# Performance work log

Measured on AMD Instinct MI355X. Metric: run time of the kernel, lower is better.

## Reference

```python
import jax, jax.numpy as jnp
import numpy as np

B, S, D = 4, 2048, 2048
H, DH = 16, 128


def setup_inputs() -> dict:
    key = jax.random.key(0)
    k1, k2, k3, k4, k5 = jax.random.split(key, 5)
    x = jax.random.normal(k1, (B, S, D), dtype=jnp.float32)
    # causal mask, broadcast over heads and batch (module does mask.unsqueeze(0))
    attn_mask = jnp.tril(jnp.ones((S, S), dtype=jnp.int32))
    # torch Linear weights: [out, in]; scaled like default init
    w_qkv = jax.random.normal(k2, (3 * H * DH, D), dtype=jnp.float32) / np.sqrt(D)
    b_qkv = jax.random.normal(k3, (3 * H * DH,), dtype=jnp.float32) * 0.01
    w_out = jax.random.normal(k4, (D, H * DH), dtype=jnp.float32) / np.sqrt(H * DH)
    b_out = jax.random.normal(k5, (D,), dtype=jnp.float32) * 0.01
    return {"x": x, "attn_mask": attn_mask, "w_qkv": w_qkv, "b_qkv": b_qkv,
            "w_out": w_out, "b_out": b_out}


def reference(x, attn_mask, w_qkv, b_qkv, w_out, b_out):
    b, s, d = x.shape
    qkv = x @ w_qkv.T + b_qkv                      # [B,S,3*H*DH]
    qkv = qkv.reshape(b, s, H, 3 * DH)             # per-head contiguous 3*DH slice
    qkv = jnp.transpose(qkv, (2, 0, 1, 3))         # [H,B,S,3*DH]
    q, k, v = jnp.split(qkv, 3, axis=-1)           # each [H,B,S,DH]
    scores = jnp.einsum('hbqd,hbkd->hbqk', q, k) / np.sqrt(DH)
    scores = jnp.where(attn_mask[None, None] == 0, -jnp.inf, scores)
    attn = jax.nn.softmax(scores, axis=-1)         # dropout is identity at eval
    ctx = jnp.einsum('hbqk,hbkd->hbqd', attn, v)   # [H,B,S,DH]
    ctx = jnp.transpose(ctx, (1, 2, 0, 3)).reshape(b, s, H * DH)
    return ctx @ w_out.T + b_out
```

## Files before the change

### kernel.cpp

```cpp
#include <hip/hip_runtime.h>

typedef unsigned short u16;
typedef __bf16 bf16x8 __attribute__((ext_vector_type(8)));
typedef unsigned short u16x8 __attribute__((ext_vector_type(8)));
typedef float f32x4 __attribute__((ext_vector_type(4)));

#define GLDS16(gp, lp)                                                        \
  __builtin_amdgcn_global_load_lds(                                           \
      (const __attribute__((address_space(1))) void*)(gp),                    \
      (__attribute__((address_space(3))) void*)(lp), 16, 0, 0)

__device__ __forceinline__ u16 f2bf(float f) {
  unsigned u = __float_as_uint(f);
  u += 0x7FFFu + ((u >> 16) & 1u);
  return (u16)(u >> 16);
}

__device__ __forceinline__ f32x4 mfma_bf16(bf16x8 a, bf16x8 b, f32x4 c) {
  return __builtin_amdgcn_mfma_f32_16x16x32_bf16(a, b, c, 0, 0, 0);
}

__global__ void cvt_f32_bf16(const float* __restrict__ src,
                             u16* __restrict__ dst, int n8) {
  for (int i = blockIdx.x * blockDim.x + threadIdx.x; i < n8;
       i += gridDim.x * blockDim.x) {
    const float4* sp = (const float4*)src + (size_t)i * 2;
    float4 a = sp[0], b = sp[1];
    u16x8 o;
    o[0] = f2bf(a.x); o[1] = f2bf(a.y); o[2] = f2bf(a.z); o[3] = f2bf(a.w);
    o[4] = f2bf(b.x); o[5] = f2bf(b.y); o[6] = f2bf(b.z); o[7] = f2bf(b.w);
    *((u16x8*)dst + i) = o;
  }
}

template <int OUT_BF16>
__global__ __launch_bounds__(512, 2) void gemm8p(const u16* __restrict__ A,
                                                 const u16* __restrict__ B,
                                                 const float* __restrict__ bias,
                                                 void* __restrict__ Cout,
                                                 int M, int N, int K, int nbm) {
  __shared__ __attribute__((aligned(16))) u16 L[2][4][8192];
  const int t = threadIdx.x, lane = t & 63, w = t >> 6;
  const int l15 = lane & 15, l4 = lane >> 4;
  const int wm = w >> 2, wn = w & 3;

  const int cpx = (int)gridDim.x >> 3;
  const int wg = (int)blockIdx.x;
  const int swz = (wg & 7) * cpx + (wg >> 3);
  const int bm = (swz % nbm) * 256;
  const int bn = (swz / nbm) * 256;

  const size_t aoff = (size_t)(t >> 3) * K + (((t & 7) ^ ((t >> 3) & 7)) << 3);
  const u16* SB[4] = {A + (size_t)bm * K, A + (size_t)(bm + 128) * K,
                      B + (size_t)bn * K, B + (size_t)(bn + 128) * K};
  const int ldst = w << 9;

#define STG(d, s, l, kt)                                                      \
  GLDS16(SB[s] + (size_t)(l) * 64 * K + (size_t)(kt) * 64 + aoff,             \
         &L[d][s][(l) * 4096 + ldst])
#define BAR __builtin_amdgcn_s_barrier()
#define WAITL asm volatile("s_waitcnt lgkmcnt(0)" ::: "memory")

  f32x4 acc[8][4];
  f32x4 z4 = {0.f, 0.f, 0.f, 0.f};
#pragma unroll
  for (int i = 0; i < 8; ++i)
#pragma unroll
    for (int j = 0; j < 4; ++j) acc[i][j] = z4;

  const u16* AH[2] = {&L[0][wm][0], &L[1][wm][0]};
  const u16* BH[2] = {&L[0][2 + (wn >> 1)][0], &L[1][2 + (wn >> 1)][0]};
  const int cb = (wn & 1) * 64;

  bf16x8 af[4][2], bfr[4][2];

  auto rdA = [&](const u16* H, int mh) {
#pragma unroll
    for (int m2 = 0; m2 < 4; ++m2) {
      int ra = mh * 64 + m2 * 16 + l15;
      const u16* p = H + ra * 64;
      af[m2][0] = *(const bf16x8*)(p + ((l4 ^ (ra & 7)) << 3));
      af[m2][1] = *(const bf16x8*)(p + (((4 + l4) ^ (ra & 7)) << 3));
    }
  };
  auto rdB = [&](const u16* H, int nh) {
#pragma unroll
    for (int n2 = 0; n2 < 2; ++n2) {
      int rb = cb + (nh * 2 + n2) * 16 + l15;
      const u16* p = H + rb * 64;
      bfr[nh * 2 + n2][0] = *(const bf16x8*)(p + ((l4 ^ (rb & 7)) << 3));
      bfr[nh * 2 + n2][1] = *(const bf16x8*)(p + (((4 + l4) ^ (rb & 7)) << 3));
    }
  };
  auto mma = [&](int mh, int nh) {
    __builtin_amdgcn_s_setprio(1);
#pragma unroll
    for (int m2 = 0; m2 < 4; ++m2)
#pragma unroll
      for (int n2 = 0; n2 < 2; ++n2) {
        int ai = mh * 4 + m2, bi = nh * 2 + n2;
        acc[ai][bi] = mfma_bf16(af[m2][0], bfr[bi][0], acc[ai][bi]);
        acc[ai][bi] = mfma_bf16(af[m2][1], bfr[bi][1], acc[ai][bi]);
      }
    __builtin_amdgcn_s_setprio(0);
  };

  STG(0, 0, 0, 0); STG(0, 0, 1, 0); STG(0, 1, 0, 0); STG(0, 1, 1, 0);
  STG(0, 2, 0, 0); STG(0, 2, 1, 0); STG(0, 3, 0, 0); STG(0, 3, 1, 0);
  STG(1, 0, 0, 1); STG(1, 1, 0, 1); STG(1, 2, 0, 1); STG(1, 2, 1, 1);
  STG(1, 3, 0, 1); STG(1, 3, 1, 1);
  asm volatile("s_waitcnt vmcnt(0)" ::: "memory");
  BAR;

  const int NI = K >> 7;
  for (int i = 0; i < NI; ++i) {
    const int kt = 2 * i;
    const bool st = (i + 1 < NI);
    rdA(AH[0], 0); rdB(BH[0], 0);
    STG(1, 0, 1, kt + 1); STG(1, 1, 1, kt + 1);
    BAR; WAITL; mma(0, 0); BAR;
    rdB(BH[0], 1);
    if (st) { STG(0, 0, 0, kt + 2); STG(0, 1, 0, kt + 2); }
    BAR; WAITL; mma(0, 1); BAR;
    rdA(AH[0], 1);
    if (st) { STG(0, 2, 0, kt + 2); STG(0, 2, 1, kt + 2); }
    BAR; WAITL; mma(1, 1); BAR;
    if (st) {
      STG(0, 3, 0, kt + 2); STG(0, 3, 1, kt + 2);
      asm volatile("s_waitcnt vmcnt(6)" ::: "memory");
    } else {
      asm volatile("s_waitcnt vmcnt(0)" ::: "memory");
    }
    BAR; mma(1, 0); BAR;
    rdA(AH[1], 0); rdB(BH[1], 0);
    if (st) { STG(0, 0, 1, kt + 2); STG(0, 1, 1, kt + 2); }
    BAR; WAITL; mma(0, 0); BAR;
    rdB(BH[1], 1);
    if (st) { STG(1, 0, 0, kt + 3); STG(1, 1, 0, kt + 3); }
    BAR; WAITL; mma(0, 1); BAR;
    rdA(AH[1], 1);
    if (st) { STG(1, 2, 0, kt + 3); STG(1, 2, 1, kt + 3); }
    BAR; WAITL; mma(1, 1); BAR;
    if (st) {
      STG(1, 3, 0, kt + 3); STG(1, 3, 1, kt + 3);
      asm volatile("s_waitcnt vmcnt(6)" ::: "memory");
    }
    BAR; mma(1, 0); BAR;
  }
#undef STG
#undef BAR
#undef WAITL

  const int cr = l4 * 4;
#pragma unroll
  for (int ni = 0; ni < 4; ++ni) {
    int col = bn + wn * 64 + ni * 16 + l15;
    float bv = bias[col];
#pragma unroll
    for (int mi = 0; mi < 8; ++mi) {
      int row = bm + wm * 128 + mi * 16 + cr;
#pragma unroll
      for (int r = 0; r < 4; ++r) {
        float v = acc[mi][ni][r] + bv;
        if (OUT_BF16)
          ((u16*)Cout)[(size_t)(row + r) * N + col] = f2bf(v);
        else
          ((float*)Cout)[(size_t)(row + r) * N + col] = v;
      }
    }
  }
}

__device__ __forceinline__ int vt_idx(int d, int kk) {
  int swz = (d ^ (d >> 3)) & 7;
  return d * 64 + ((((kk >> 3) ^ swz) << 3) | (kk & 7));
}
__device__ __forceinline__ int ps_idx(int r, int c) {
  return r * 64 + ((((c >> 3) ^ ((r >> 2) & 7)) << 3) | (c & 7));
}

__global__ __launch_bounds__(256, 2) void attn_fwd(const u16* __restrict__ qkv,
                                                   u16* __restrict__ ctx) {
  constexpr int NQ = 6144, SD = 2048;
  __shared__ __attribute__((aligned(16))) u16 Ks[2][64 * 128];
  __shared__ __attribute__((aligned(16))) u16 Vt[2][128 * 64];
  __shared__ __attribute__((aligned(16))) u16 Ps[128 * 64];
  const int t = threadIdx.x, lane = t & 63, w = t >> 6;
  const int l15 = lane & 15, l4 = lane >> 4;
  const int h = blockIdx.y, b = blockIdx.z;
  const size_t rowbase = (size_t)b * 2048;
  const int hq = h * 384;

  const u16* Kg = qkv + (rowbase + (t >> 4)) * NQ + hq + 128 +
                  (((t & 15) ^ ((t >> 4) & 7)) << 3);
  const u16* Vg = qkv + (rowbase + (t & 15)) * NQ + hq + 256 + ((t >> 4) << 3);
  const int vkk = t & 15, vd0 = (t >> 4) << 3;

  const float C = 0.12751879522447905f;
  const float THRC = 62.73592239488341f;

  for (int seg = 0; seg < 2; ++seg) {
    const int qt = (seg == 0) ? (15 - (int)blockIdx.x) : (int)blockIdx.x;
    const int q0 = qt * 128;
    const int nt = 2 * qt + 2;
    const int qr0 = q0 + w * 32 + l4 * 4;

    bf16x8 qf[2][4];
#pragma unroll
    for (int mi = 0; mi < 2; ++mi) {
      const u16* qp =
          qkv + (rowbase + q0 + w * 32 + mi * 16 + l15) * NQ + hq + l4 * 8;
#pragma unroll
      for (int kc = 0; kc < 4; ++kc) qf[mi][kc] = *(const bf16x8*)(qp + kc * 32);
    }

    f32x4 z4 = {0.f, 0.f, 0.f, 0.f};
    f32x4 oacc[2][8];
#pragma unroll
    for (int mi = 0; mi < 2; ++mi)
#pragma unroll
      for (int i = 0; i < 8; ++i) oacc[mi][i] = z4;
    float m_run[2][4], l_run[2][4];
#pragma unroll
    for (int mi = 0; mi < 2; ++mi)
#pragma unroll
      for (int r = 0; r < 4; ++r) { m_run[mi][r] = -3.0e38f; l_run[mi][r] = 0.f; }

    u16x8 vA[4], vB[4];
#pragma unroll
    for (int i = 0; i < 4; ++i)
      GLDS16(Kg + (size_t)(i * 16) * NQ, &Ks[0][i * 2048 + w * 512]);
#pragma unroll
    for (int p = 0; p < 4; ++p)
      vA[p] = *(const u16x8*)(Vg + (size_t)(p * 16) * NQ);
    __syncthreads();
#pragma unroll
    for (int p = 0; p < 4; ++p) {
      int kk = p * 16 + vkk;
#pragma unroll
      for (int j = 0; j < 8; ++j) Vt[0][vt_idx(vd0 + j, kk)] = vA[p][j];
    }
#pragma unroll
    for (int p = 0; p < 4; ++p)
      vA[p] = *(const u16x8*)(Vg + (size_t)(64 + p * 16) * NQ);
    __syncthreads();

    for (int tt = 0; tt < nt; ++tt) {
      const int k0 = tt * 64, cur = tt & 1;
      const int kn = (k0 + 64 < q0 + 64) ? k0 + 64 : q0 + 64;
#pragma unroll
      for (int i = 0; i < 4; ++i)
        GLDS16(Kg + (size_t)(kn + i * 16) * NQ,
               &Ks[cur ^ 1][i * 2048 + w * 512]);
      const int kv = (k0 + 128 < q0 + 64) ? k0 + 128 : q0 + 64;
#pragma unroll
      for (int p = 0; p < 4; ++p)
        vB[p] = *(const u16x8*)(Vg + (size_t)(kv + p * 16) * NQ);

      f32x4 sc[2][4];
#pragma unroll
      for (int mi = 0; mi < 2; ++mi)
#pragma unroll
        for (int nf = 0; nf < 4; ++nf) sc[mi][nf] = z4;
#pragma unroll
      for (int kc = 0; kc < 4; ++kc)
#pragma unroll
        for (int nf = 0; nf < 4; ++nf) {
          int rk = nf * 16 + l15;
          bf16x8 kf = *(const bf16x8*)(&Ks[cur][rk * 128 +
                                              (((kc * 4 + l4) ^ (rk & 7)) << 3)]);
          sc[0][nf] = mfma_bf16(qf[0][kc], kf, sc[0][nf]);
          sc[1][nf] = mfma_bf16(qf[1][kc], kf, sc[1][nf]);
        }
      if (tt + 2 >= nt) {
#pragma unroll
        for (int mi = 0; mi < 2; ++mi)
#pragma unroll
          for (int nf = 0; nf < 4; ++nf) {
            int col = k0 + nf * 16 + l15;
            int qr = qr0 + mi * 16;
#pragma unroll
            for (int r = 0; r < 4; ++r)
              if (col > qr + r) sc[mi][nf][r] = -3.0e38f;
          }
      }
      float mx[2][4];
#pragma unroll
      for (int mi = 0; mi < 2; ++mi)
#pragma unroll
        for (int r = 0; r < 4; ++r)
          mx[mi][r] = fmaxf(fmaxf(sc[mi][0][r], sc[mi][1][r]),
                            fmaxf(sc[mi][2][r], sc[mi][3][r]));
#pragma unroll
      for (int off = 8; off >= 1; off >>= 1)
#pragma unroll
        for (int mi = 0; mi < 2; ++mi)
#pragma unroll
          for (int r = 0; r < 4; ++r)
            mx[mi][r] = fmaxf(mx[mi][r], __shfl_xor(mx[mi][r], off));
      bool upd = false;
#pragma unroll
      for (int mi = 0; mi < 2; ++mi)
#pragma unroll
        for (int r = 0; r < 4; ++r)
          upd |= (mx[mi][r] > m_run[mi][r] + THRC);
      if (__any(upd)) {
#pragma unroll
        for (int mi = 0; mi < 2; ++mi)
#pragma unroll
          for (int r = 0; r < 4; ++r) {
            float mn = fmaxf(m_run[mi][r], mx[mi][r]);
            float cr = exp2f((m_run[mi][r] - mn) * C);
            m_run[mi][r] = mn;
            l_run[mi][r] *= cr;
#pragma unroll
            for (int nf = 0; nf < 8; ++nf) oacc[mi][nf][r] *= cr;
          }
      }
#pragma unroll
      for (int mi = 0; mi < 2; ++mi) {
        float mC[4], sm[4];
#pragma unroll
        for (int r = 0; r < 4; ++r) mC[r] = m_run[mi][r] * C;
#pragma unroll
        for (int nf = 0; nf < 4; ++nf)
#pragma unroll
          for (int r = 0; r < 4; ++r)
            sc[mi][nf][r] = exp2f(fmaf(sc[mi][nf][r], C, -mC[r]));
#pragma unroll
        for (int r = 0; r < 4; ++r)
          sm[r] = (sc[mi][0][r] + sc[mi][1][r]) + (sc[mi][2][r] + sc[mi][3][r]);
#pragma unroll
        for (int off = 8; off >= 1; off >>= 1)
#pragma unroll
          for (int r = 0; r < 4; ++r) sm[r] += __shfl_xor(sm[r], off);
#pragma unroll
        for (int r = 0; r < 4; ++r) l_run[mi][r] += sm[r];
#pragma unroll
        for (int nf = 0; nf < 4; ++nf)
#pragma unroll
          for (int r = 0; r < 4; ++r)
            ((__bf16*)Ps)[ps_idx(w * 32 + mi * 16 + l4 * 4 + r,
                                 nf * 16 + l15)] = (__bf16)sc[mi][nf][r];
      }
#pragma unroll
      for (int p = 0; p < 4; ++p) {
        int kk = p * 16 + vkk;
#pragma unroll
        for (int j = 0; j < 8; ++j) Vt[cur ^ 1][vt_idx(vd0 + j, kk)] = vA[p][j];
      }
#pragma unroll
      for (int kc = 0; kc < 2; ++kc) {
        bf16x8 pf0 =
            *(const bf16x8*)(Ps + ps_idx(w * 32 + l15, kc * 32 + l4 * 8));
        bf16x8 pf1 =
            *(const bf16x8*)(Ps + ps_idx(w * 32 + 16 + l15, kc * 32 + l4 * 8));
#pragma unroll
        for (int nf = 0; nf < 8; ++nf) {
          bf16x8 vf = *(const bf16x8*)(&Vt[cur][vt_idx(nf * 16 + l15,
                                                       kc * 32 + l4 * 8)]);
          oacc[0][nf] = mfma_bf16(pf0, vf, oacc[0][nf]);
          oacc[1][nf] = mfma_bf16(pf1, vf, oacc[1][nf]);
        }
      }
      __syncthreads();
#pragma unroll
      for (int p = 0; p < 4; ++p) vA[p] = vB[p];
    }
#pragma unroll
    for (int mi = 0; mi < 2; ++mi) {
      float inv[4];
#pragma unroll
      for (int r = 0; r < 4; ++r) inv[r] = 1.f / l_run[mi][r];
      u16* cp = ctx + (rowbase + q0 + w * 32 + mi * 16 + l4 * 4) * SD +
                h * 128 + l15;
#pragma unroll
      for (int nf = 0; nf < 8; ++nf)
#pragma unroll
        for (int r = 0; r < 4; ++r)
          ((__bf16*)cp)[(size_t)r * SD + nf * 16] =
              (__bf16)(oacc[mi][nf][r] * inv[r]);
    }
  }
}

extern "C" void kernel_launch(void* const* d_in, const int* in_sizes, int n_in,
                              void* d_out, int out_size, void* d_ws,
                              size_t ws_size, hipStream_t stream) {
  const float* x = (const float*)d_in[0];
  const float* wqkv = (const float*)d_in[2];
  const float* bqkv = (const float*)d_in[3];
  const float* wout = (const float*)d_in[4];
  const float* bout = (const float*)d_in[5];
  float* out = (float*)d_out;
  char* ws = (char*)d_ws;

  u16* xb = (u16*)(ws);
  u16* wqkvb = (u16*)(ws + 33554432);
  u16* woutb = (u16*)(ws + 58720256);
  u16* qkvb = (u16*)(ws + 67108864);
  u16* ctx = xb;

  cvt_f32_bf16<<<2048, 256, 0, stream>>>(x, xb, 16777216 / 8);
  cvt_f32_bf16<<<2048, 256, 0, stream>>>(wqkv, wqkvb, 12582912 / 8);
  cvt_f32_bf16<<<1024, 256, 0, stream>>>(wout, woutb, 4194304 / 8);
  gemm8p<1><<<dim3(32 * 24), 512, 0, stream>>>(xb, wqkvb, bqkv, qkvb, 8192,
                                               6144, 2048, 32);
  attn_fwd<<<dim3(8, 16, 4), 256, 0, stream>>>(qkvb, ctx);
  gemm8p<0><<<dim3(32 * 8), 512, 0, stream>>>(ctx, woutb, bout, out, 8192,
                                              2048, 2048, 32);
}
```

Baseline: 635.7 us.

## Single-buffer attention LDS, one q-tile per block, raise occupancy to three

The attention kernel drops double-buffered K/V shared memory and the async global-to-LDS K load. It now loads K and V through registers and stores them into single LDS buffers with an extra barrier per tile. Each block handles one query tile, longest first, instead of pairing two tiles, so the grid becomes 1024 blocks and launch bounds rise to 3 waves per SIMD. The aim is higher occupancy and better load balance through scheduling, at the cost of less intra-block load/compute overlap and more synchronisation.

```diff
diff --git a/kernel.cpp b/kernel.cpp
--- a/kernel.cpp
+++ b/kernel.cpp
@@ -179,208 +179,212 @@
   return r * 64 + ((((c >> 3) ^ ((r >> 2) & 7)) << 3) | (c & 7));
 }
 
-__global__ __launch_bounds__(256, 2) void attn_fwd(const u16* __restrict__ qkv,
+__global__ __launch_bounds__(256, 3) void attn_fwd(const u16* __restrict__ qkv,
                                                    u16* __restrict__ ctx) {
   constexpr int NQ = 6144, SD = 2048;
-  __shared__ __attribute__((aligned(16))) u16 Ks[2][64 * 128];
-  __shared__ __attribute__((aligned(16))) u16 Vt[2][128 * 64];
+  __shared__ __attribute__((aligned(16))) u16 Ks[64 * 128];
+  __shared__ __attribute__((aligned(16))) u16 Vt[128 * 64];
   __shared__ __attribute__((aligned(16))) u16 Ps[128 * 64];
   const int t = threadIdx.x, lane = t & 63, w = t >> 6;
   const int l15 = lane & 15, l4 = lane >> 4;
-  const int h = blockIdx.y, b = blockIdx.z;
+
+  const int L = (int)blockIdx.x;
+  const int qt = 15 - (L >> 6);
+  const int h = L & 15, b = (L >> 4) & 3;
   const size_t rowbase = (size_t)b * 2048;
   const int hq = h * 384;
-
-  const u16* Kg = qkv + (rowbase + (t >> 4)) * NQ + hq + 128 +
-                  (((t & 15) ^ ((t >> 4) & 7)) << 3);
+  const int q0 = qt * 128;
+  const int nt = 2 * qt + 2;
+  const int qr0 = q0 + w * 32 + l4 * 4;
+
+  const u16* KgR =
+      qkv + (rowbase + (t >> 4)) * NQ + hq + 128 + ((t & 15) << 3);
+  const int krow0 = t >> 4;
+  const int kslot = ((t & 15) ^ ((t >> 4) & 7)) << 3;
   const u16* Vg = qkv + (rowbase + (t & 15)) * NQ + hq + 256 + ((t >> 4) << 3);
   const int vkk = t & 15, vd0 = (t >> 4) << 3;
 
   const float C = 0.12751879522447905f;
   const float THRC = 62.73592239488341f;
 
-  for (int seg = 0; seg < 2; ++seg) {
-    const int qt = (seg == 0) ? (15 - (int)blockIdx.x) : (int)blockIdx.x;
-    const int q0 = qt * 128;
-    const int nt = 2 * qt + 2;
-    const int qr0 = q0 + w * 32 + l4 * 4;
-
-    bf16x8 qf[2][4];
+  bf16x8 qf[2][4];
+#pragma unroll
+  for (int mi = 0; mi < 2; ++mi) {
+    const u16* qp =
+        qkv + (rowbase + q0 + w * 32 + mi * 16 + l15) * NQ + hq + l4 * 8;
+#pragma unroll
+    for (int kc = 0; kc < 4; ++kc) qf[mi][kc] = *(const bf16x8*)(qp + kc * 32);
+  }
+
+  f32x4 z4 = {0.f, 0.f, 0.f, 0.f};
+  f32x4 oacc[2][8];
+#pragma unroll
+  for (int mi = 0; mi < 2; ++mi)
+#pragma unroll
+    for (int i = 0; i < 8; ++i) oacc[mi][i] = z4;
+  float m_run[2][4], l_run[2][4];
+#pragma unroll
+  for (int mi = 0; mi < 2; ++mi)
+#pragma unroll
+    for (int r = 0; r < 4; ++r) { m_run[mi][r] = -3.0e38f; l_run[mi][r] = 0.f; }
+
+  u16x8 kA[4], vA[4];
+#pragma unroll
+  for (int i = 0; i < 4; ++i)
+    kA[i] = *(const u16x8*)(KgR + (size_t)(i * 16) * NQ);
+#pragma unroll
+  for (int p = 0; p < 4; ++p)
+    vA[p] = *(const u16x8*)(Vg + (size_t)(p * 16) * NQ);
+#pragma unroll
+  for (int i = 0; i < 4; ++i)
+    *(u16x8*)(Ks + (i * 16 + krow0) * 128 + kslot) = kA[i];
+#pragma unroll
+  for (int p = 0; p < 4; ++p) {
+    int kk = p * 16 + vkk;
+#pragma unroll
+    for (int j = 0; j < 8; ++j) Vt[vt_idx(vd0 + j, kk)] = vA[p][j];
+  }
+  __syncthreads();
+
+  for (int tt = 0; tt < nt; ++tt) {
+    const int k0 = tt * 64;
+    const bool more = (tt + 1 < nt);
+
+    f32x4 sc[2][4];
+#pragma unroll
+    for (int mi = 0; mi < 2; ++mi)
+#pragma unroll
+      for (int nf = 0; nf < 4; ++nf) sc[mi][nf] = z4;
+#pragma unroll
+    for (int kc = 0; kc < 4; ++kc)
+#pragma unroll
+      for (int nf = 0; nf < 4; ++nf) {
+        int rk = nf * 16 + l15;
+        bf16x8 kf = *(const bf16x8*)(Ks + rk * 128 +
+                                     (((kc * 4 + l4) ^ (rk & 7)) << 3));
+        sc[0][nf] = mfma_bf16(qf[0][kc], kf, sc[0][nf]);
+        sc[1][nf] = mfma_bf16(qf[1][kc], kf, sc[1][nf]);
+      }
+    if (tt + 2 >= nt) {
+#pragma unroll
+      for (int mi = 0; mi < 2; ++mi)
+#pragma unroll
+        for (int nf = 0; nf < 4; ++nf) {
+          int col = k0 + nf * 16 + l15;
+          int qr = qr0 + mi * 16;
+#pragma unroll
+          for (int r = 0; r < 4; ++r)
+            if (col > qr + r) sc[mi][nf][r] = -3.0e38f;
+        }
+    }
+    float mx[2][4];
+#pragma unroll
+    for (int mi = 0; mi < 2; ++mi)
+#pragma unroll
+      for (int r = 0; r < 4; ++r)
+        mx[mi][r] = fmaxf(fmaxf(sc[mi][0][r], sc[mi][1][r]),
+                          fmaxf(sc[mi][2][r], sc[mi][3][r]));
+#pragma unroll
+    for (int off = 8; off >= 1; off >>= 1)
+#pragma unroll
+      for (int mi = 0; mi < 2; ++mi)
+#pragma unroll
+        for (int r = 0; r < 4; ++r)
+          mx[mi][r] = fmaxf(mx[mi][r], __shfl_xor(mx[mi][r], off));
+    bool upd = false;
+#pragma unroll
+    for (int mi = 0; mi < 2; ++mi)
+#pragma unroll
+      for (int r = 0; r < 4; ++r) upd |= (mx[mi][r] > m_run[mi][r] + THRC);
+    if (__any(upd)) {
+#pragma unroll
+      for (int mi = 0; mi < 2; ++mi)
+#pragma unroll
+        for (int r = 0; r < 4; ++r) {
+          float mn = fmaxf(m_run[mi][r], mx[mi][r]);
+          float cr = exp2f((m_run[mi][r] - mn) * C);
+          m_run[mi][r] = mn;
+          l_run[mi][r] *= cr;
+#pragma unroll
+          for (int nf = 0; nf < 8; ++nf) oacc[mi][nf][r] *= cr;
+        }
+    }
 #pragma unroll
     for (int mi = 0; mi < 2; ++mi) {
-      const u16* qp =
-          qkv + (rowbase + q0 + w * 32 + mi * 16 + l15) * NQ + hq + l4 * 8;
-#pragma unroll
-      for (int kc = 0; kc < 4; ++kc) qf[mi][kc] = *(const bf16x8*)(qp + kc * 32);
-    }
-
-    f32x4 z4 = {0.f, 0.f, 0.f, 0.f};
-    f32x4 oacc[2][8];
-#pragma unroll
-    for (int mi = 0; mi < 2; ++mi)
-#pragma unroll
-      for (int i = 0; i < 8; ++i) oacc[mi][i] = z4;
-    float m_run[2][4], l_run[2][4];
-#pragma unroll
-    for (int mi = 0; mi < 2; ++mi)
-#pragma unroll
-      for (int r = 0; r < 4; ++r) { m_run[mi][r] = -3.0e38f; l_run[mi][r] = 0.f; }
-
-    u16x8 vA[4], vB[4];
-#pragma unroll
-    for (int i = 0; i < 4; ++i)
-      GLDS16(Kg + (size_t)(i * 16) * NQ, &Ks[0][i * 2048 + w * 512]);
-#pragma unroll
-    for (int p = 0; p < 4; ++p)
-      vA[p] = *(const u16x8*)(Vg + (size_t)(p * 16) * NQ);
-    __syncthreads();
-#pragma unroll
-    for (int p = 0; p < 4; ++p) {
-      int kk = p * 16 + vkk;
-#pragma unroll
-      for (int j = 0; j < 8; ++j) Vt[0][vt_idx(vd0 + j, kk)] = vA[p][j];
-    }
-#pragma unroll
-    for (int p = 0; p < 4; ++p)
-      vA[p] = *(const u16x8*)(Vg + (size_t)(64 + p * 16) * NQ);
-    __syncthreads();
-
-    for (int tt = 0; tt < nt; ++tt) {
-      const int k0 = tt * 64, cur = tt & 1;
-      const int kn = (k0 + 64 < q0 + 64) ? k0 + 64 : q0 + 64;
+      float mC[4], sm[4];
+#pragma unroll
+      for (int r = 0; r < 4; ++r) mC[r] = m_run[mi][r] * C;
+#pragma unroll
+      for (int nf = 0; nf < 4; ++nf)
+#pragma unroll
+        for (int r = 0; r < 4; ++r)
+          sc[mi][nf][r] = exp2f(fmaf(sc[mi][nf][r], C, -mC[r]));
+#pragma unroll
+      for (int r = 0; r < 4; ++r)
+        sm[r] = (sc[mi][0][r] + sc[mi][1][r]) + (sc[mi][2][r] + sc[mi][3][r]);
+#pragma unroll
+      for (int off = 8; off >= 1; off >>= 1)
+#pragma unroll
+        for (int r = 0; r < 4; ++r) sm[r] += __shfl_xor(sm[r], off);
+#pragma unroll
+      for (int r = 0; r < 4; ++r) l_run[mi][r] += sm[r];
+#pragma unroll
+      for (int nf = 0; nf < 4; ++nf)
+#pragma unroll
+        for (int r = 0; r < 4; ++r)
+          ((__bf16*)Ps)[ps_idx(w * 32 + mi * 16 + l4 * 4 + r,
+                               nf * 16 + l15)] = (__bf16)sc[mi][nf][r];
+    }
+    if (more) {
+      const int knl = (tt + 1) * 64;
 #pragma unroll
       for (int i = 0; i < 4; ++i)
-        GLDS16(Kg + (size_t)(kn + i * 16) * NQ,
-               &Ks[cur ^ 1][i * 2048 + w * 512]);
-      const int kv = (k0 + 128 < q0 + 64) ? k0 + 128 : q0 + 64;
+        kA[i] = *(const u16x8*)(KgR + (size_t)(knl + i * 16) * NQ);
 #pragma unroll
       for (int p = 0; p < 4; ++p)
-        vB[p] = *(const u16x8*)(Vg + (size_t)(kv + p * 16) * NQ);
-
-      f32x4 sc[2][4];
-#pragma unroll
-      for (int mi = 0; mi < 2; ++mi)
-#pragma unroll
-        for (int nf = 0; nf < 4; ++nf) sc[mi][nf] = z4;
-#pragma unroll
-      for (int kc = 0; kc < 4; ++kc)
-#pragma unroll
-        for (int nf = 0; nf < 4; ++nf) {
-          int rk = nf * 16 + l15;
-          bf16x8 kf = *(const bf16x8*)(&Ks[cur][rk * 128 +
-                                              (((kc * 4 + l4) ^ (rk & 7)) << 3)]);
-          sc[0][nf] = mfma_bf16(qf[0][kc], kf, sc[0][nf]);
-          sc[1][nf] = mfma_bf16(qf[1][kc], kf, sc[1][nf]);
-        }
-      if (tt + 2 >= nt) {
-#pragma unroll
-        for (int mi = 0; mi < 2; ++mi)
-#pragma unroll
-          for (int nf = 0; nf < 4; ++nf) {
-            int col = k0 + nf * 16 + l15;
-            int qr = qr0 + mi * 16;
-#pragma unroll
-            for (int r = 0; r < 4; ++r)
-              if (col > qr + r) sc[mi][nf][r] = -3.0e38f;
-          }
+        vA[p] = *(const u16x8*)(Vg + (size_t)(knl + p * 16) * NQ);
+    }
+#pragma unroll
+    for (int kc = 0; kc < 2; ++kc) {
+      bf16x8 pf0 =
+          *(const bf16x8*)(Ps + ps_idx(w * 32 + l15, kc * 32 + l4 * 8));
+      bf16x8 pf1 =
+          *(const bf16x8*)(Ps + ps_idx(w * 32 + 16 + l15, kc * 32 + l4 * 8));
+#pragma unroll
+      for (int nf = 0; nf < 8; ++nf) {
+        bf16x8 vf =
+            *(const bf16x8*)(Vt + vt_idx(nf * 16 + l15, kc * 32 + l4 * 8));
+        oacc[0][nf] = mfma_bf16(pf0, vf, oacc[0][nf]);
+        oacc[1][nf] = mfma_bf16(pf1, vf, oacc[1][nf]);
       }
-      float mx[2][4];
-#pragma unroll
-      for (int mi = 0; mi < 2; ++mi)
-#pragma unroll
-        for (int r = 0; r < 4; ++r)
-          mx[mi][r] = fmaxf(fmaxf(sc[mi][0][r], sc[mi][1][r]),
-                            fmaxf(sc[mi][2][r], sc[mi][3][r]));
-#pragma unroll
-      for (int off = 8; off >= 1; off >>= 1)
-#pragma unroll
-        for (int mi = 0; mi < 2; ++mi)
-#pragma unroll
-          for (int r = 0; r < 4; ++r)
-            mx[mi][r] = fmaxf(mx[mi][r], __shfl_xor(mx[mi][r], off));
-      bool upd = false;
-#pragma unroll
-      for (int mi = 0; mi < 2; ++mi)
-#pragma unroll
-        for (int r = 0; r < 4; ++r)
-          upd |= (mx[mi][r] > m_run[mi][r] + THRC);
-      if (__any(upd)) {
-#pragma unroll
-        for (int mi = 0; mi < 2; ++mi)
-#pragma unroll
-          for (int r = 0; r < 4; ++r) {
-            float mn = fmaxf(m_run[mi][r], mx[mi][r]);
-            float cr = exp2f((m_run[mi][r] - mn) * C);
-            m_run[mi][r] = mn;
-            l_run[mi][r] *= cr;
-#pragma unroll
-            for (int nf = 0; nf < 8; ++nf) oacc[mi][nf][r] *= cr;
-          }
-      }
-#pragma unroll
-      for (int mi = 0; mi < 2; ++mi) {
-        float mC[4], sm[4];
-#pragma unroll
-        for (int r = 0; r < 4; ++r) mC[r] = m_run[mi][r] * C;
-#pragma unroll
-        for (int nf = 0; nf < 4; ++nf)
-#pragma unroll
-          for (int r = 0; r < 4; ++r)
-            sc[mi][nf][r] = exp2f(fmaf(sc[mi][nf][r], C, -mC[r]));
-#pragma unroll
-        for (int r = 0; r < 4; ++r)
-          sm[r] = (sc[mi][0][r] + sc[mi][1][r]) + (sc[mi][2][r] + sc[mi][3][r]);
-#pragma unroll
-        for (int off = 8; off >= 1; off >>= 1)
-#pragma unroll
-          for (int r = 0; r < 4; ++r) sm[r] += __shfl_xor(sm[r], off);
-#pragma unroll
-        for (int r = 0; r < 4; ++r) l_run[mi][r] += sm[r];
-#pragma unroll
-        for (int nf = 0; nf < 4; ++nf)
-#pragma unroll
-          for (int r = 0; r < 4; ++r)
-            ((__bf16*)Ps)[ps_idx(w * 32 + mi * 16 + l4 * 4 + r,
-                                 nf * 16 + l15)] = (__bf16)sc[mi][nf][r];
-      }
+    }
+    if (more) {
+      __syncthreads();
+#pragma unroll
+      for (int i = 0; i < 4; ++i)
+        *(u16x8*)(Ks + (i * 16 + krow0) * 128 + kslot) = kA[i];
 #pragma unroll
       for (int p = 0; p < 4; ++p) {
         int kk = p * 16 + vkk;
 #pragma unroll
-        for (int j = 0; j < 8; ++j) Vt[cur ^ 1][vt_idx(vd0 + j, kk)] = vA[p][j];
-      }
-#pragma unroll
-      for (int kc = 0; kc < 2; ++kc) {
-        bf16x8 pf0 =
-            *(const bf16x8*)(Ps + ps_idx(w * 32 + l15, kc * 32 + l4 * 8));
-        bf16x8 pf1 =
-            *(const bf16x8*)(Ps + ps_idx(w * 32 + 16 + l15, kc * 32 + l4 * 8));
-#pragma unroll
-        for (int nf = 0; nf < 8; ++nf) {
-          bf16x8 vf = *(const bf16x8*)(&Vt[cur][vt_idx(nf * 16 + l15,
-                                                       kc * 32 + l4 * 8)]);
-          oacc[0][nf] = mfma_bf16(pf0, vf, oacc[0][nf]);
-          oacc[1][nf] = mfma_bf16(pf1, vf, oacc[1][nf]);
-        }
+        for (int j = 0; j < 8; ++j) Vt[vt_idx(vd0 + j, kk)] = vA[p][j];
       }
       __syncthreads();
-#pragma unroll
-      for (int p = 0; p < 4; ++p) vA[p] = vB[p];
-    }
-#pragma unroll
-    for (int mi = 0; mi < 2; ++mi) {
-      float inv[4];
-#pragma unroll
-      for (int r = 0; r < 4; ++r) inv[r] = 1.f / l_run[mi][r];
-      u16* cp = ctx + (rowbase + q0 + w * 32 + mi * 16 + l4 * 4) * SD +
-                h * 128 + l15;
-#pragma unroll
-      for (int nf = 0; nf < 8; ++nf)
-#pragma unroll
-        for (int r = 0; r < 4; ++r)
-          ((__bf16*)cp)[(size_t)r * SD + nf * 16] =
-              (__bf16)(oacc[mi][nf][r] * inv[r]);
-    }
+    }
+  }
+#pragma unroll
+  for (int mi = 0; mi < 2; ++mi) {
+    float inv[4];
+#pragma unroll
+    for (int r = 0; r < 4; ++r) inv[r] = 1.f / l_run[mi][r];
+    u16* cp = ctx + (rowbase + q0 + w * 32 + mi * 16 + l4 * 4) * SD +
+              h * 128 + l15;
+#pragma unroll
+    for (int nf = 0; nf < 8; ++nf)
+#pragma unroll
+      for (int r = 0; r < 4; ++r)
+        ((__bf16*)cp)[(size_t)r * SD + nf * 16] =
+            (__bf16)(oacc[mi][nf][r] * inv[r]);
   }
 }
 
@@ -406,7 +410,7 @@
   cvt_f32_bf16<<<1024, 256, 0, stream>>>(wout, woutb, 4194304 / 8);
   gemm8p<1><<<dim3(32 * 24), 512, 0, stream>>>(xb, wqkvb, bqkv, qkvb, 8192,
                                                6144, 2048, 32);
-  attn_fwd<<<dim3(8, 16, 4), 256, 0, stream>>>(qkvb, ctx);
+  attn_fwd<<<dim3(1024), 256, 0, stream>>>(qkvb, ctx);
   gemm8p<0><<<dim3(32 * 8), 512, 0, stream>>>(ctx, woutb, bout, out, 8192,
                                               2048, 2048, 32);
 }
```

After: 979.4 us. 1.54x slower.
